# Kernel optimization log

Measured on AMD Instinct MI355X. Metric: run time of the kernel, lower is better.

Reference implementation:

```python
import jax, jax.numpy as jnp
import numpy as np

ONE_STEP = 14
EPS = 1e-5


def _bn(x, g, b):
    # training-mode batchnorm over the node/batch axis (biased variance)
    m = jnp.mean(x, axis=0)
    v = jnp.var(x, axis=0)
    return (x - m) * jax.lax.rsqrt(v + EPS) * g + b


def _gcn_conv(x, W, b, src, dst, dis):
    N = x.shape[0]
    h = x @ W
    norm = (dis[src] * dis[dst])[:, None]
    agg = jax.ops.segment_sum(h[src] * norm, dst, num_segments=N)
    agg = agg + (dis * dis)[:, None] * h  # self-loop contribution
    return agg + b


def setup_inputs() -> dict:
    key = jax.random.key(0)
    ks = jax.random.split(key, 16)
    N, F, E, NC = 114688, 512, 917504, 10
    x = jax.random.normal(ks[0], (N, F), jnp.float32)
    edge_index = jax.random.randint(ks[1], (2, E), 0, N, jnp.int32)

    def lin(k, i, o):
        return jax.random.normal(k, (i, o), jnp.float32) / np.sqrt(i).astype(np.float32)

    d = {"x": x, "edge_index": edge_index}
    dims = [(F, 128), (128, 256), (256, 64), (64, 32)]
    for li, (i, o) in enumerate(dims, 1):
        d[f"W{li}"] = lin(ks[1 + li], i, o)
        d[f"b{li}"] = jnp.zeros((o,), jnp.float32)
        d[f"bn{li}_g"] = jnp.ones((o,), jnp.float32)
        d[f"bn{li}_b"] = jnp.zeros((o,), jnp.float32)
    d["gW1"] = lin(ks[6], 32, 16); d["gb1"] = jnp.zeros((16,), jnp.float32)
    d["gbn1_g"] = jnp.ones((16,), jnp.float32); d["gbn1_b"] = jnp.zeros((16,), jnp.float32)
    d["gW2"] = lin(ks[7], 16, 1); d["gb2"] = jnp.zeros((1,), jnp.float32)
    d["gbn2_g"] = jnp.ones((1,), jnp.float32); d["gbn2_b"] = jnp.zeros((1,), jnp.float32)
    d["fcW"] = lin(ks[8], 32, NC); d["fcb"] = jnp.zeros((NC,), jnp.float32)
    return d


def reference(x, edge_index, W1, b1, bn1_g, bn1_b, W2, b2, bn2_g, bn2_b,
              W3, b3, bn3_g, bn3_b, W4, b4, bn4_g, bn4_b,
              gW1, gb1, gbn1_g, gbn1_b, gW2, gb2, gbn2_g, gbn2_b, fcW, fcb):
    N = x.shape[0]
    src, dst = edge_index[0], edge_index[1]
    # degree with self-loops (counted on dst, per PyG gcn_norm)
    deg = jax.ops.segment_sum(jnp.ones_like(dst, jnp.float32), dst, num_segments=N) + 1.0
    dis = jax.lax.rsqrt(deg)

    h = _bn(jax.nn.relu(_gcn_conv(x, W1, b1, src, dst, dis)), bn1_g, bn1_b)
    h = _bn(jax.nn.relu(_gcn_conv(h, W2, b2, src, dst, dis)), bn2_g, bn2_b)
    h = _bn(jax.nn.relu(_gcn_conv(h, W3, b3, src, dst, dis)), bn3_g, bn3_b)
    h = _bn(jax.nn.relu(_gcn_conv(h, W4, b4, src, dst, dis)), bn4_g, bn4_b)

    # gate network: Linear -> BN -> ReLU -> Linear -> BN -> ReLU
    g = jax.nn.relu(_bn(h @ gW1 + gb1, gbn1_g, gbn1_b))
    g = jax.nn.relu(_bn(g @ gW2 + gb2, gbn2_g, gbn2_b))[:, 0]  # [N]

    B = N // ONE_STEP
    batch = jnp.repeat(jnp.arange(B), ONE_STEP)
    # segment softmax over nodes of each graph
    m = jax.ops.segment_max(g, batch, num_segments=B)
    e = jnp.exp(g - m[batch])
    s = jax.ops.segment_sum(e, batch, num_segments=B)
    alpha = e / s[batch]
    pooled = jax.ops.segment_sum(alpha[:, None] * h, batch, num_segments=B)  # [B,32]

    # dropout is identity in eval mode
    logits = pooled @ fcW + fcb
    return jax.nn.softmax(logits, axis=1)
```

## Files before the change

### kernel.cpp

```cpp
#include <hip/hip_runtime.h>

#define NN 114688
#define NE 917504
#define NBATCH 8192
#define GSZ 14
#define NCLS 10
#define EPSB 1e-5f
#define NSCAN 112

typedef unsigned short u16;
typedef short bf16x8 __attribute__((ext_vector_type(8)));
typedef float f32x4 __attribute__((ext_vector_type(4)));
typedef _Float16 h8t __attribute__((ext_vector_type(8)));
typedef unsigned short u16x8 __attribute__((ext_vector_type(8)));

__device__ __forceinline__ float bf2f(u16 u) {
    union { unsigned int i; float f; } v; v.i = ((unsigned int)u) << 16; return v.f;
}
__device__ __forceinline__ u16 f2bf(float f) {
    union { float f; unsigned int i; } v; v.f = f;
    unsigned int i = v.i;
    unsigned int r = i + 0x7FFFu + ((i >> 16) & 1u);
    return (u16)(r >> 16);
}
__device__ __forceinline__ void splitbf(float y, u16& h, u16& l) {
    h = f2bf(y);
    l = f2bf(y - bf2f(h));
}

__global__ __launch_bounds__(256) void k_hist(const int* __restrict__ ei, int* __restrict__ counts) {
    int e = blockIdx.x * 256 + threadIdx.x;
    atomicAdd(&counts[ei[NE + e]], 1);
}

__global__ __launch_bounds__(256) void k_scan1(const int* __restrict__ counts, int* __restrict__ bsum) {
    __shared__ int red[256];
    int tid = threadIdx.x;
    int base = blockIdx.x * 1024 + tid * 4;
    int s = counts[base] + counts[base + 1] + counts[base + 2] + counts[base + 3];
    red[tid] = s; __syncthreads();
    for (int o = 128; o > 0; o >>= 1) {
        if (tid < o) red[tid] += red[tid + o];
        __syncthreads();
    }
    if (tid == 0) bsum[blockIdx.x] = red[0];
}

__global__ void k_scan2(int* bsum, int* offs) {
    if (threadIdx.x == 0) {
        int run = 0;
        for (int i = 0; i < NSCAN; i++) { int t = bsum[i]; bsum[i] = run; run += t; }
        offs[NN] = run;
    }
}

__global__ __launch_bounds__(256) void k_scan3(const int* __restrict__ counts, const int* __restrict__ bsum,
                                               int* __restrict__ offs) {
    __shared__ int ss[256];
    int tid = threadIdx.x;
    int base = blockIdx.x * 1024 + tid * 4;
    int v0 = counts[base], v1 = counts[base + 1], v2 = counts[base + 2], v3 = counts[base + 3];
    int ts = v0 + v1 + v2 + v3;
    ss[tid] = ts; __syncthreads();
    for (int o = 1; o < 256; o <<= 1) {
        int add = (tid >= o) ? ss[tid - o] : 0;
        __syncthreads();
        ss[tid] += add;
        __syncthreads();
    }
    int excl = ss[tid] - ts + bsum[blockIdx.x];
    offs[base] = excl;
    offs[base + 1] = excl + v0;
    offs[base + 2] = excl + v0 + v1;
    offs[base + 3] = excl + v0 + v1 + v2;
}

__global__ __launch_bounds__(256) void k_dis_cursor(const int* __restrict__ counts, const int* __restrict__ offs,
                                                    float* __restrict__ dis, int* __restrict__ cursor) {
    int n = blockIdx.x * 256 + threadIdx.x;
    dis[n] = rsqrtf((float)counts[n] + 1.0f);
    cursor[n] = offs[n];
}

__global__ __launch_bounds__(256) void k_scatter(const int* __restrict__ ei, int* __restrict__ cursor,
                                                 int* __restrict__ srcs, float* __restrict__ sd,
                                                 const float* __restrict__ dis, float* __restrict__ wsa) {
    int e = blockIdx.x * 256 + threadIdx.x;
    int d = ei[NE + e], s = ei[e];
    int p = atomicAdd(&cursor[d], 1);
    float w = dis[s];
    srcs[p] = s;
    sd[p] = w;
    atomicAdd(&wsa[d], w);
}

__global__ __launch_bounds__(256) void k_tsplit(const float* __restrict__ Wsrc,
                                                u16* __restrict__ Wh, u16* __restrict__ Wl,
                                                int K, int F) {
    int i = blockIdx.x * 256 + threadIdx.x;
    if (i < K * F) {
        int k = i / F, f = i % F;
        u16 h, l; splitbf(Wsrc[i], h, l);
        Wh[f * K + k] = h;
        Wl[f * K + k] = l;
    }
}

__global__ __launch_bounds__(256) void k_wsplit(const float* __restrict__ W, const float* __restrict__ sc,
                                                u16* __restrict__ Wh, u16* __restrict__ Wl,
                                                int K, int F) {
    int i = blockIdx.x * 256 + threadIdx.x;
    if (i < K * F) {
        int k = i / F, f = i % F;
        u16 h, l; splitbf(sc[k] * W[i], h, l);
        Wh[f * K + k] = h;
        Wl[f * K + k] = l;
    }
}

__global__ __launch_bounds__(256) void k_wc2(const float* __restrict__ W, const float* __restrict__ sh,
                                             float* __restrict__ c2, int K, int F) {
    int wv = (blockIdx.x * 256 + threadIdx.x) >> 6;
    int lane = threadIdx.x & 63;
    if (wv >= F) return;
    float acc = 0.f;
    for (int k = lane; k < K; k += 64) acc += sh[k] * W[k * F + wv];
#pragma unroll
    for (int o = 1; o < 64; o <<= 1) acc += __shfl_xor(acc, o);
    if (lane == 0) c2[wv] = acc;
}

template<int BM, int BN, int WCOLS, bool AFP32, bool C2, bool TEPI>
__global__ __launch_bounds__(256) void k_gemm(
    const float* __restrict__ Af, const u16* __restrict__ Ahi, const u16* __restrict__ Alo,
    const u16* __restrict__ Wh, const u16* __restrict__ Wl,
    _Float16* __restrict__ C, const int K, const int Fout, const float* __restrict__ c2,
    const float* __restrict__ bias, const float* __restrict__ wsa, const float* __restrict__ disv,
    u16* __restrict__ Thi, u16* __restrict__ Tlo, float* __restrict__ Sg, float* __restrict__ Qg)
{
    constexpr int AST = 40;
    __shared__ u16 Ah[BM][AST], Al[BM][AST];
    __shared__ u16 Bh[BN][AST], Bl[BN][AST];
    __shared__ float redS[TEPI ? BN : 1], redQ[TEPI ? BN : 1];

    const int tid = threadIdx.x;
    const int row0 = blockIdx.y * BM;
    const int col0 = blockIdx.x * BN;

    const int wave = tid >> 6, lane = tid & 63;
    const int mb = (wave / WCOLS) * 64;
    const int nb = (wave % WCOLS) * 64;
    const int lm = lane & 15;
    const int lk = (lane >> 4) * 8;
    const int cb = col0 + nb + lm;

    if constexpr (TEPI) {
        for (int i = tid; i < BN; i += 256) { redS[i] = 0.f; redQ[i] = 0.f; }
    }

    float c2v[4] = {0.f, 0.f, 0.f, 0.f};
    if constexpr (C2) {
#pragma unroll
        for (int ni = 0; ni < 4; ni++) c2v[ni] = c2[cb + ni * 16];
    }

    f32x4 acc[4][4];
#pragma unroll
    for (int i = 0; i < 4; i++)
#pragma unroll
        for (int j = 0; j < 4; j++)
#pragma unroll
            for (int r = 0; r < 4; r++) acc[i][j][r] = c2v[j];

    const int stg_r = tid >> 3;
    const int stg_c = (tid & 7) * 4;

    for (int k0 = 0; k0 < K; k0 += 32) {
        __syncthreads();
#pragma unroll
        for (int p = 0; p < BM / 32; p++) {
            const int r = p * 32 + stg_r;
            if constexpr (AFP32) {
                const float4 v = *(const float4*)(Af + (size_t)(row0 + r) * K + k0 + stg_c);
                float y[4] = {v.x, v.y, v.z, v.w};
                ushort4 hv, lv;
#pragma unroll
                for (int q = 0; q < 4; q++) splitbf(y[q], ((u16*)&hv)[q], ((u16*)&lv)[q]);
                *(ushort4*)&Ah[r][stg_c] = hv;
                *(ushort4*)&Al[r][stg_c] = lv;
            } else {
                *(ushort4*)&Ah[r][stg_c] = *(const ushort4*)(Ahi + (size_t)(row0 + r) * K + k0 + stg_c);
                *(ushort4*)&Al[r][stg_c] = *(const ushort4*)(Alo + (size_t)(row0 + r) * K + k0 + stg_c);
            }
        }
#pragma unroll
        for (int p = 0; p < BN / 32; p++) {
            const int n = p * 32 + stg_r;
            *(ushort4*)&Bh[n][stg_c] = *(const ushort4*)(Wh + (size_t)(col0 + n) * K + k0 + stg_c);
            *(ushort4*)&Bl[n][stg_c] = *(const ushort4*)(Wl + (size_t)(col0 + n) * K + k0 + stg_c);
        }
        __syncthreads();

        bf16x8 ah[4], al[4], bh[4], bl[4];
#pragma unroll
        for (int mi = 0; mi < 4; mi++) {
            ah[mi] = *(const bf16x8*)&Ah[mb + mi * 16 + lm][lk];
            al[mi] = *(const bf16x8*)&Al[mb + mi * 16 + lm][lk];
        }
#pragma unroll
        for (int ni = 0; ni < 4; ni++) {
            bh[ni] = *(const bf16x8*)&Bh[nb + ni * 16 + lm][lk];
            bl[ni] = *(const bf16x8*)&Bl[nb + ni * 16 + lm][lk];
        }
#pragma unroll
        for (int mi = 0; mi < 4; mi++)
#pragma unroll
            for (int ni = 0; ni < 4; ni++) {
                acc[mi][ni] = __builtin_amdgcn_mfma_f32_16x16x32_bf16(al[mi], bh[ni], acc[mi][ni], 0, 0, 0);
                acc[mi][ni] = __builtin_amdgcn_mfma_f32_16x16x32_bf16(ah[mi], bl[ni], acc[mi][ni], 0, 0, 0);
                acc[mi][ni] = __builtin_amdgcn_mfma_f32_16x16x32_bf16(ah[mi], bh[ni], acc[mi][ni], 0, 0, 0);
            }
    }

    const int rb = row0 + mb + (lane >> 4) * 4;
    if constexpr (TEPI) {
        float c2l[4], bl4[4];
#pragma unroll
        for (int ni = 0; ni < 4; ni++) { c2l[ni] = c2[cb + ni * 16]; bl4[ni] = bias[cb + ni * 16]; }
        float ws[4][4];
#pragma unroll
        for (int mi = 0; mi < 4; mi++)
#pragma unroll
            for (int r = 0; r < 4; r++) {
                const int row = rb + mi * 16 + r;
                const float d = disv[row];
                ws[mi][r] = d * wsa[row] + d * d;
            }
#pragma unroll
        for (int ni = 0; ni < 4; ni++) {
            float s = 0.f, q = 0.f;
#pragma unroll
            for (int mi = 0; mi < 4; mi++)
#pragma unroll
                for (int r = 0; r < 4; r++) {
                    float v = acc[mi][ni][r] + ws[mi][r] * c2l[ni] + bl4[ni];
                    v = fmaxf(v, 0.f);
                    s += v; q += v * v;
                    u16 hh, ll; splitbf(v, hh, ll);
                    const size_t idx = (size_t)(rb + mi * 16 + r) * Fout + cb + ni * 16;
                    Thi[idx] = hh;
                    Tlo[idx] = ll;
                }
            atomicAdd(&redS[nb + ni * 16 + lm], s);
            atomicAdd(&redQ[nb + ni * 16 + lm], q);
        }
        __syncthreads();
        for (int i = tid; i < BN; i += 256) {
            atomicAdd(&Sg[col0 + i], redS[i]);
            atomicAdd(&Qg[col0 + i], redQ[i]);
        }
    } else {
#pragma unroll
        for (int mi = 0; mi < 4; mi++)
#pragma unroll
            for (int ni = 0; ni < 4; ni++)
#pragma unroll
                for (int r = 0; r < 4; r++)
                    C[(size_t)(rb + mi * 16 + r) * Fout + cb + ni * 16] = (_Float16)acc[mi][ni][r];
    }
}

template<int CH, bool FP16OUT>
__global__ __launch_bounds__(256) void k_agg(
    const _Float16* __restrict__ h, u16* __restrict__ thi, u16* __restrict__ tlo,
    const float* __restrict__ bias,
    const int* __restrict__ off, const int* __restrict__ srcs, const float* __restrict__ sd,
    const float* __restrict__ dis, float* __restrict__ statS, float* __restrict__ statQ,
    _Float16* __restrict__ tf)
{
    constexpr int ECH = 16;
    constexpr int LPG = CH / ECH;
    constexpr int G   = 64 / LPG;
    constexpr int NB  = NN / G;
    __shared__ float redS[CH], redQ[CH];
    const int tid = threadIdx.x;
    for (int i = tid; i < CH; i += 256) { redS[i] = 0.f; redQ[i] = 0.f; }
    __syncthreads();

    const int lane = tid & 63;
    const int g = lane / LPG;
    const int c = (lane % LPG) * ECH;
    const int wid = (blockIdx.x * 256 + tid) >> 6;
    const int nw = (gridDim.x * 256) >> 6;

    float bs[ECH], bq[ECH], bv[ECH];
#pragma unroll
    for (int v = 0; v < ECH; v++) { bs[v] = 0.f; bq[v] = 0.f; bv[v] = bias[c + v]; }

    for (int b = wid; b < NB; b += nw) {
        const int n = b * G + g;
        const int p0 = off[n], p1 = off[n + 1];
        float a[ECH];
#pragma unroll
        for (int v = 0; v < ECH; v++) a[v] = 0.f;

        int p = p0;
        int s = 0; float w = 0.f;
        if (p < p1) { s = srcs[p]; w = sd[p]; }
        while (p < p1) {
            int s2 = 0; float w2 = 0.f;
            if (p + 1 < p1) { s2 = srcs[p + 1]; w2 = sd[p + 1]; }
            const _Float16* hr = h + (size_t)s * CH + c;
            h8t hv0 = *(const h8t*)hr;
            h8t hv1 = *(const h8t*)(hr + 8);
#pragma unroll
            for (int v = 0; v < 8; v++) { a[v] += w * (float)hv0[v]; a[v + 8] += w * (float)hv1[v]; }
            s = s2; w = w2; ++p;
        }
        const float dn = dis[n];
        const float dn2 = dn * dn;
        const _Float16* hr = h + (size_t)n * CH + c;
        h8t hn0 = *(const h8t*)hr;
        h8t hn1 = *(const h8t*)(hr + 8);
        float o16[ECH];
#pragma unroll
        for (int v = 0; v < 8; v++) {
            o16[v] = fmaxf(dn * a[v] + dn2 * (float)hn0[v] + bv[v], 0.f);
            o16[v + 8] = fmaxf(dn * a[v + 8] + dn2 * (float)hn1[v] + bv[v + 8], 0.f);
        }
#pragma unroll
        for (int v = 0; v < ECH; v++) { bs[v] += o16[v]; bq[v] += o16[v] * o16[v]; }
        if constexpr (FP16OUT) {
            h8t o0, o1;
#pragma unroll
            for (int v = 0; v < 8; v++) { o0[v] = (_Float16)o16[v]; o1[v] = (_Float16)o16[v + 8]; }
            _Float16* tr = tf + (size_t)n * CH + c;
            *(h8t*)tr = o0; *(h8t*)(tr + 8) = o1;
        } else {
            u16x8 hv0, lv0, hv1, lv1;
#pragma unroll
            for (int v = 0; v < 8; v++) {
                splitbf(o16[v], ((u16*)&hv0)[v], ((u16*)&lv0)[v]);
                splitbf(o16[v + 8], ((u16*)&hv1)[v], ((u16*)&lv1)[v]);
            }
            u16* th = thi + (size_t)n * CH + c;
            u16* tl = tlo + (size_t)n * CH + c;
            *(u16x8*)th = hv0; *(u16x8*)(th + 8) = hv1;
            *(u16x8*)tl = lv0; *(u16x8*)(tl + 8) = lv1;
        }
    }
#pragma unroll
    for (int o = LPG; o < 64; o <<= 1) {
#pragma unroll
        for (int v = 0; v < ECH; v++) { bs[v] += __shfl_xor(bs[v], o); bq[v] += __shfl_xor(bq[v], o); }
    }
    if (g == 0) {
#pragma unroll
        for (int v = 0; v < ECH; v++) { atomicAdd(&redS[c + v], bs[v]); atomicAdd(&redQ[c + v], bq[v]); }
    }
    __syncthreads();
    for (int i = tid; i < CH; i += 256) { atomicAdd(&statS[i], redS[i]); atomicAdd(&statQ[i], redQ[i]); }
}

template<int CH>
__global__ __launch_bounds__(256) void k_agglin(
    const _Float16* __restrict__ t, u16* __restrict__ uhi, u16* __restrict__ ulo,
    const int* __restrict__ off, const int* __restrict__ srcs, const float* __restrict__ sd,
    const float* __restrict__ dis)
{
    constexpr int ECH = 16;
    constexpr int LPG = CH / ECH;
    constexpr int G   = 64 / LPG;
    constexpr int NB  = NN / G;
    const int tid = threadIdx.x;
    const int lane = tid & 63;
    const int g = lane / LPG;
    const int c = (lane % LPG) * ECH;
    const int wid = (blockIdx.x * 256 + tid) >> 6;
    const int nw = (gridDim.x * 256) >> 6;

    for (int b = wid; b < NB; b += nw) {
        const int n = b * G + g;
        const int p0 = off[n], p1 = off[n + 1];
        float a[ECH];
#pragma unroll
        for (int v = 0; v < ECH; v++) a[v] = 0.f;

        int p = p0;
        int s = 0; float w = 0.f;
        if (p < p1) { s = srcs[p]; w = sd[p]; }
        while (p < p1) {
            int s2 = 0; float w2 = 0.f;
            if (p + 1 < p1) { s2 = srcs[p + 1]; w2 = sd[p + 1]; }
            const _Float16* hr = t + (size_t)s * CH + c;
            h8t hv0 = *(const h8t*)hr;
            h8t hv1 = *(const h8t*)(hr + 8);
#pragma unroll
            for (int v = 0; v < 8; v++) { a[v] += w * (float)hv0[v]; a[v + 8] += w * (float)hv1[v]; }
            s = s2; w = w2; ++p;
        }
        const float dn = dis[n];
        const float dn2 = dn * dn;
        const _Float16* hr = t + (size_t)n * CH + c;
        h8t hn0 = *(const h8t*)hr;
        h8t hn1 = *(const h8t*)(hr + 8);
        u16x8 hv0, lv0, hv1, lv1;
#pragma unroll
        for (int v = 0; v < 8; v++) {
            float o0 = dn * a[v] + dn2 * (float)hn0[v];
            float o1 = dn * a[v + 8] + dn2 * (float)hn1[v];
            splitbf(o0, ((u16*)&hv0)[v], ((u16*)&lv0)[v]);
            splitbf(o1, ((u16*)&hv1)[v], ((u16*)&lv1)[v]);
        }
        u16* th = uhi + (size_t)n * CH + c;
        u16* tl = ulo + (size_t)n * CH + c;
        *(u16x8*)th = hv0; *(u16x8*)(th + 8) = hv1;
        *(u16x8*)tl = lv0; *(u16x8*)(tl + 8) = lv1;
    }
}

__global__ void k_bnpar(const float* __restrict__ S, const float* __restrict__ Q,
                        const float* __restrict__ g, const float* __restrict__ b,
                        float* __restrict__ sc, float* __restrict__ sh, int F) {
    int c = threadIdx.x;
    if (c >= F) return;
    const float invn = 1.0f / (float)NN;
    float mean = S[c] * invn;
    float var = Q[c] * invn - mean * mean;
    float s = g[c] * rsqrtf(fmaxf(var, 0.f) + EPSB);
    sc[c] = s;
    sh[c] = b[c] - mean * s;
}

template<int K, int F, bool BIAS, bool STATS>
__global__ __launch_bounds__(256) void k_smm(
    const u16* __restrict__ Ahi, const u16* __restrict__ Alo,
    const float* __restrict__ Wf, const float* __restrict__ bias,
    _Float16* __restrict__ C, const float* __restrict__ sc, const float* __restrict__ sh,
    float* __restrict__ Sg, float* __restrict__ Qg)
{
    __shared__ float Wl[K * F];
    __shared__ float scl[K], shl[K], bl[F];
    __shared__ float redS[F], redQ[F];
    const int tid = threadIdx.x;
    for (int i = tid; i < K * F; i += 256) Wl[i] = Wf[i];
    if (tid < K) { scl[tid] = sc[tid]; shl[tid] = sh[tid]; }
    if (tid < F) {
        bl[tid] = 0.f;
        if constexpr (BIAS) bl[tid] = bias[tid];
        if constexpr (STATS) { redS[tid] = 0.f; redQ[tid] = 0.f; }
    }
    __syncthreads();
    const int n = blockIdx.x * 256 + tid;
    float acc[F];
#pragma unroll
    for (int f = 0; f < F; f++) acc[f] = bl[f];
    const u16* ah = Ahi + (size_t)n * K;
    const u16* al = Alo + (size_t)n * K;
    for (int k = 0; k < K; k += 4) {
        ushort4 hv = *(const ushort4*)(ah + k);
        ushort4 lv = *(const ushort4*)(al + k);
        float y0 = (bf2f(hv.x) + bf2f(lv.x)) * scl[k] + shl[k];
        float y1 = (bf2f(hv.y) + bf2f(lv.y)) * scl[k + 1] + shl[k + 1];
        float y2 = (bf2f(hv.z) + bf2f(lv.z)) * scl[k + 2] + shl[k + 2];
        float y3 = (bf2f(hv.w) + bf2f(lv.w)) * scl[k + 3] + shl[k + 3];
#pragma unroll
        for (int f = 0; f < F; f += 4) {
            float4 w0 = *(const float4*)&Wl[k * F + f];
            float4 w1 = *(const float4*)&Wl[(k + 1) * F + f];
            float4 w2 = *(const float4*)&Wl[(k + 2) * F + f];
            float4 w3 = *(const float4*)&Wl[(k + 3) * F + f];
            acc[f + 0] += y0 * w0.x + y1 * w1.x + y2 * w2.x + y3 * w3.x;
            acc[f + 1] += y0 * w0.y + y1 * w1.y + y2 * w2.y + y3 * w3.y;
            acc[f + 2] += y0 * w0.z + y1 * w1.z + y2 * w2.z + y3 * w3.z;
            acc[f + 3] += y0 * w0.w + y1 * w1.w + y2 * w2.w + y3 * w3.w;
        }
    }
    _Float16* cr = C + (size_t)n * F;
#pragma unroll
    for (int f = 0; f < F; f++) cr[f] = (_Float16)acc[f];
    if constexpr (STATS) {
        float s[F], q[F];
#pragma unroll
        for (int f = 0; f < F; f++) { s[f] = acc[f]; q[f] = acc[f] * acc[f]; }
#pragma unroll
        for (int o = 1; o < 64; o <<= 1) {
#pragma unroll
            for (int f = 0; f < F; f++) { s[f] += __shfl_xor(s[f], o); q[f] += __shfl_xor(q[f], o); }
        }
        if ((tid & 63) == 0) {
#pragma unroll
            for (int f = 0; f < F; f++) { atomicAdd(&redS[f], s[f]); atomicAdd(&redQ[f], q[f]); }
        }
        __syncthreads();
        for (int i = tid; i < F; i += 256) { atomicAdd(&Sg[i], redS[i]); atomicAdd(&Qg[i], redQ[i]); }
    }
}

__global__ __launch_bounds__(256) void k_gate2(const _Float16* __restrict__ g1,
                                               const float* __restrict__ sc, const float* __restrict__ sh,
                                               const float* __restrict__ w2, const float* __restrict__ b2,
                                               float* __restrict__ g2,
                                               float* __restrict__ Sg, float* __restrict__ Qg) {
    __shared__ float wl[16], scl[16], shl[16], b2l[1];
    __shared__ float redSg[1], redQg[1];
    const int tid = threadIdx.x;
    if (tid < 16) { wl[tid] = w2[tid]; scl[tid] = sc[tid]; shl[tid] = sh[tid]; }
    if (tid == 0) { b2l[0] = b2[0]; redSg[0] = 0.f; redQg[0] = 0.f; }
    __syncthreads();
    const int n = blockIdx.x * 256 + tid;
    const _Float16* r = g1 + (size_t)n * 16;
    float acc = b2l[0];
#pragma unroll
    for (int k = 0; k < 16; k++) {
        float y = fmaxf((float)r[k] * scl[k] + shl[k], 0.f);
        acc += y * wl[k];
    }
    g2[n] = acc;
    float s = acc, q = acc * acc;
#pragma unroll
    for (int o = 1; o < 64; o <<= 1) { s += __shfl_xor(s, o); q += __shfl_xor(q, o); }
    if ((tid & 63) == 0) { atomicAdd(&redSg[0], s); atomicAdd(&redQg[0], q); }
    __syncthreads();
    if (tid == 0) { atomicAdd(&Sg[0], redSg[0]); atomicAdd(&Qg[0], redQg[0]); }
}

__global__ __launch_bounds__(256) void k_pool(const u16* __restrict__ t4hi, const u16* __restrict__ t4lo,
                                              const float* __restrict__ sc4, const float* __restrict__ sh4,
                                              const float* __restrict__ g2,
                                              const float* __restrict__ gsc2, const float* __restrict__ gsh2,
                                              const float* __restrict__ fcW, const float* __restrict__ fcb,
                                              float* __restrict__ out) {
    __shared__ float fw[32 * NCLS], fbl[NCLS], sc4l[32], sh4l[32];
    const int tid = threadIdx.x;
    for (int i = tid; i < 32 * NCLS; i += 256) fw[i] = fcW[i];
    if (tid < NCLS) fbl[tid] = fcb[tid];
    if (tid < 32) { sc4l[tid] = sc4[tid]; sh4l[tid] = sh4[tid]; }
    __syncthreads();
    const int b = blockIdx.x * 256 + tid;
    const float s2 = gsc2[0], h2 = gsh2[0];
    const int base = b * GSZ;

    float gv[GSZ];
    float m = -1e30f;
#pragma unroll
    for (int i = 0; i < GSZ; i++) {
        float v = fmaxf(g2[base + i] * s2 + h2, 0.f);
        gv[i] = v; m = fmaxf(m, v);
    }
    float ssum = 0.f;
#pragma unroll
    for (int i = 0; i < GSZ; i++) { float e = __expf(gv[i] - m); gv[i] = e; ssum += e; }
    const float inv = 1.0f / ssum;

    float pooled[32];
#pragma unroll
    for (int c = 0; c < 32; c++) pooled[c] = 0.f;
#pragma unroll
    for (int i = 0; i < GSZ; i++) {
        const float a = gv[i] * inv;
        const u16* th = t4hi + (size_t)(base + i) * 32;
        const u16* tl = t4lo + (size_t)(base + i) * 32;
#pragma unroll
        for (int c = 0; c < 32; c += 4) {
            ushort4 hv = *(const ushort4*)(th + c);
            ushort4 lv = *(const ushort4*)(tl + c);
            pooled[c + 0] += a * ((bf2f(hv.x) + bf2f(lv.x)) * sc4l[c + 0] + sh4l[c + 0]);
            pooled[c + 1] += a * ((bf2f(hv.y) + bf2f(lv.y)) * sc4l[c + 1] + sh4l[c + 1]);
            pooled[c + 2] += a * ((bf2f(hv.z) + bf2f(lv.z)) * sc4l[c + 2] + sh4l[c + 2]);
            pooled[c + 3] += a * ((bf2f(hv.w) + bf2f(lv.w)) * sc4l[c + 3] + sh4l[c + 3]);
        }
    }
    float lg[NCLS];
    float mx = -1e30f;
#pragma unroll
    for (int j = 0; j < NCLS; j++) {
        float a = fbl[j];
#pragma unroll
        for (int c = 0; c < 32; c++) a += pooled[c] * fw[c * NCLS + j];
        lg[j] = a; mx = fmaxf(mx, a);
    }
    float es = 0.f;
#pragma unroll
    for (int j = 0; j < NCLS; j++) { float e = __expf(lg[j] - mx); lg[j] = e; es += e; }
    const float iv = 1.0f / es;
#pragma unroll
    for (int j = 0; j < NCLS; j++) out[b * NCLS + j] = lg[j] * iv;
}

extern "C" void kernel_launch(void* const* d_in, const int* in_sizes, int n_in,
                              void* d_out, int out_size, void* d_ws, size_t ws_size,
                              hipStream_t stream) {
    (void)in_sizes; (void)n_in; (void)out_size; (void)ws_size;
    const float* x    = (const float*)d_in[0];
    const int*   ei   = (const int*)d_in[1];
    const float* W1   = (const float*)d_in[2];
    const float* b1   = (const float*)d_in[3];
    const float* bn1g = (const float*)d_in[4];
    const float* bn1b = (const float*)d_in[5];
    const float* W2   = (const float*)d_in[6];
    const float* b2   = (const float*)d_in[7];
    const float* bn2g = (const float*)d_in[8];
    const float* bn2b = (const float*)d_in[9];
    const float* W3   = (const float*)d_in[10];
    const float* b3   = (const float*)d_in[11];
    const float* bn3g = (const float*)d_in[12];
    const float* bn3b = (const float*)d_in[13];
    const float* W4   = (const float*)d_in[14];
    const float* b4   = (const float*)d_in[15];
    const float* bn4g = (const float*)d_in[16];
    const float* bn4b = (const float*)d_in[17];
    const float* gW1  = (const float*)d_in[18];
    const float* gb1  = (const float*)d_in[19];
    const float* gbn1g = (const float*)d_in[20];
    const float* gbn1b = (const float*)d_in[21];
    const float* gW2  = (const float*)d_in[22];
    const float* gb2  = (const float*)d_in[23];
    const float* gbn2g = (const float*)d_in[24];
    const float* gbn2b = (const float*)d_in[25];
    const float* fcW  = (const float*)d_in[26];
    const float* fcb  = (const float*)d_in[27];
    float* out = (float*)d_out;

    char* base = (char*)d_ws;
    size_t off_ = 0;
    auto carve = [&](size_t bytes) -> char* {
        char* p = base + off_;
        off_ = (off_ + bytes + 255) & ~(size_t)255;
        return p;
    };
    int*   counts = (int*)carve((size_t)NN * 4);
    float* stats  = (float*)carve(994 * 4);
    float* wsa    = (float*)carve((size_t)NN * 4);
    const size_t zero_bytes = off_;
    int*   offs   = (int*)carve((size_t)(NN + 1) * 4);
    int*   cursor = (int*)carve((size_t)NN * 4);
    int*   srcs   = (int*)carve((size_t)NE * 4);
    float* sd     = (float*)carve((size_t)NE * 4);
    float* dis    = (float*)carve((size_t)NN * 4);
    int*   bsum   = (int*)carve(NSCAN * 4);
    float* pars   = (float*)carve(994 * 4);
    u16*   Wt1h   = (u16*)carve(512 * 128 * 2);
    u16*   Wt1l   = (u16*)carve(512 * 128 * 2);
    u16*   Wt2h   = (u16*)carve(128 * 256 * 2);
    u16*   Wt2l   = (u16*)carve(128 * 256 * 2);
    u16*   Wt3h   = (u16*)carve(256 * 64 * 2);
    u16*   Wt3l   = (u16*)carve(256 * 64 * 2);
    float* c2_2   = (float*)carve(256 * 4);
    float* c2_3   = (float*)carve(64 * 4);
    float* g2raw  = (float*)carve((size_t)NN * 4);
    _Float16* P   = (_Float16*)carve((size_t)NN * 256 * 2);
    u16*   Qhi    = (u16*)carve((size_t)NN * 128 * 2);
    u16*   Qlo    = (u16*)carve((size_t)NN * 128 * 2);
    u16*   Rhi    = (u16*)carve((size_t)NN * 256 * 2);
    u16*   Rlo    = (u16*)carve((size_t)NN * 256 * 2);
    _Float16* T1f = P + (size_t)NN * 128;

    float* S1 = stats;      float* Q1s = S1 + 128;
    float* S2 = Q1s + 128;  float* Q2s = S2 + 256;
    float* S3 = Q2s + 256;  float* Q3s = S3 + 64;
    float* S4 = Q3s + 64;   float* Q4s = S4 + 32;
    float* gS1 = Q4s + 32;  float* gQ1 = gS1 + 16;
    float* gS2 = gQ1 + 16;  float* gQ2 = gS2 + 1;

    float* sc1 = pars;      float* sh1 = sc1 + 128;
    float* sc2 = sh1 + 128; float* sh2 = sc2 + 256;
    float* sc3 = sh2 + 256; float* sh3 = sc3 + 64;
    float* sc4 = sh3 + 64;  float* sh4 = sc4 + 32;
    float* gsc1 = sh4 + 32; float* gsh1 = gsc1 + 16;
    float* gsc2 = gsh1 + 16; float* gsh2 = gsc2 + 1;

    hipMemsetAsync(d_ws, 0, zero_bytes, stream);

    k_hist<<<NE / 256, 256, 0, stream>>>(ei, counts);
    k_scan1<<<NSCAN, 256, 0, stream>>>(counts, bsum);
    k_scan2<<<1, 64, 0, stream>>>(bsum, offs);
    k_scan3<<<NSCAN, 256, 0, stream>>>(counts, bsum, offs);
    k_dis_cursor<<<NN / 256, 256, 0, stream>>>(counts, offs, dis, cursor);
    k_scatter<<<NE / 256, 256, 0, stream>>>(ei, cursor, srcs, sd, dis, wsa);
    k_tsplit<<<(512 * 128 + 255) / 256, 256, 0, stream>>>(W1, Wt1h, Wt1l, 512, 128);

    k_gemm<128, 128, 2, true, false, false><<<dim3(1, NN / 128), 256, 0, stream>>>(
        x, nullptr, nullptr, Wt1h, Wt1l, P, 512, 128, nullptr,
        nullptr, nullptr, nullptr, nullptr, nullptr, nullptr, nullptr);
    k_agg<128, true><<<1792, 256, 0, stream>>>(P, nullptr, nullptr, b1, offs, srcs, sd, dis, S1, Q1s, T1f);
    k_bnpar<<<1, 256, 0, stream>>>(S1, Q1s, bn1g, bn1b, sc1, sh1, 128);

    k_agglin<128><<<1792, 256, 0, stream>>>(T1f, Qhi, Qlo, offs, srcs, sd, dis);
    k_wsplit<<<(128 * 256 + 255) / 256, 256, 0, stream>>>(W2, sc1, Wt2h, Wt2l, 128, 256);
    k_wc2<<<(256 * 64 + 255) / 256, 256, 0, stream>>>(W2, sh1, c2_2, 128, 256);
    k_gemm<128, 128, 2, false, false, true><<<dim3(2, NN / 128), 256, 0, stream>>>(
        nullptr, Qhi, Qlo, Wt2h, Wt2l, nullptr, 128, 256, c2_2,
        b2, wsa, dis, Rhi, Rlo, S2, Q2s);
    k_bnpar<<<1, 256, 0, stream>>>(S2, Q2s, bn2g, bn2b, sc2, sh2, 256);

    k_wsplit<<<(256 * 64 + 255) / 256, 256, 0, stream>>>(W3, sc2, Wt3h, Wt3l, 256, 64);
    k_wc2<<<(64 * 64 + 255) / 256, 256, 0, stream>>>(W3, sh2, c2_3, 256, 64);
    k_gemm<256, 64, 1, false, true, false><<<dim3(1, NN / 256), 256, 0, stream>>>(
        nullptr, Rhi, Rlo, Wt3h, Wt3l, P, 256, 64, c2_3,
        nullptr, nullptr, nullptr, nullptr, nullptr, nullptr, nullptr);
    k_agg<64, false><<<1792, 256, 0, stream>>>(P, Qhi, Qlo, b3, offs, srcs, sd, dis, S3, Q3s, nullptr);
    k_bnpar<<<1, 256, 0, stream>>>(S3, Q3s, bn3g, bn3b, sc3, sh3, 64);

    k_smm<64, 32, false, false><<<NN / 256, 256, 0, stream>>>(Qhi, Qlo, W4, nullptr, P, sc3, sh3,
                                                              nullptr, nullptr);
    k_agg<32, false><<<896, 256, 0, stream>>>(P, Qhi, Qlo, b4, offs, srcs, sd, dis, S4, Q4s, nullptr);
    k_bnpar<<<1, 256, 0, stream>>>(S4, Q4s, bn4g, bn4b, sc4, sh4, 32);

    k_smm<32, 16, true, true><<<NN / 256, 256, 0, stream>>>(Qhi, Qlo, gW1, gb1, P, sc4, sh4, gS1, gQ1);
    k_bnpar<<<1, 256, 0, stream>>>(gS1, gQ1, gbn1g, gbn1b, gsc1, gsh1, 16);

    k_gate2<<<NN / 256, 256, 0, stream>>>(P, gsc1, gsh1, gW2, gb2, g2raw, gS2, gQ2);
    k_bnpar<<<1, 256, 0, stream>>>(gS2, gQ2, gbn2g, gbn2b, gsc2, gsh2, 1);

    k_pool<<<NBATCH / 256, 256, 0, stream>>>(Qhi, Qlo, sc4, sh4, g2raw, gsc2, gsh2, fcW, fcb, out);
}
```

Baseline: 974.9 us.

## Fold BN parameter kernels into consumers, fuse dis/cursor into scan, unroll gather

Removes the six tiny k_bnpar launches by computing batchnorm scale/shift inline in each consuming kernel from the raw sum and sum-of-squares. It also folds the dis/cursor initialisation into k_scan3, and unrolls the edge-gather loops in the aggregation kernels by two so each iteration has two independent row loads in flight. The goal is fewer kernel launches and more memory-level parallelism in the gathers. In exchange, some BN parameter math is recomputed redundantly per thread, for example inside k_wsplit and k_wc2.

```diff
diff --git a/kernel.cpp b/kernel.cpp
--- a/kernel.cpp
+++ b/kernel.cpp
@@ -26,6 +26,16 @@
 __device__ __forceinline__ void splitbf(float y, u16& h, u16& l) {
     h = f2bf(y);
     l = f2bf(y - bf2f(h));
+}
+__device__ __forceinline__ void bnparams(const float* __restrict__ S, const float* __restrict__ Q,
+                                         const float* __restrict__ g, const float* __restrict__ b,
+                                         int c, float& sc, float& sh) {
+    const float invn = 1.0f / (float)NN;
+    float mean = S[c] * invn;
+    float var = Q[c] * invn - mean * mean;
+    float s = g[c] * rsqrtf(fmaxf(var, 0.f) + EPSB);
+    sc = s;
+    sh = b[c] - mean * s;
 }
 
 __global__ __launch_bounds__(256) void k_hist(const int* __restrict__ ei, int* __restrict__ counts) {
@@ -55,7 +65,8 @@
 }
 
 __global__ __launch_bounds__(256) void k_scan3(const int* __restrict__ counts, const int* __restrict__ bsum,
-                                               int* __restrict__ offs) {
+                                               int* __restrict__ offs, float* __restrict__ dis,
+                                               int* __restrict__ cursor) {
     __shared__ int ss[256];
     int tid = threadIdx.x;
     int base = blockIdx.x * 1024 + tid * 4;
@@ -69,17 +80,13 @@
         __syncthreads();
     }
     int excl = ss[tid] - ts + bsum[blockIdx.x];
-    offs[base] = excl;
-    offs[base + 1] = excl + v0;
-    offs[base + 2] = excl + v0 + v1;
-    offs[base + 3] = excl + v0 + v1 + v2;
-}
-
-__global__ __launch_bounds__(256) void k_dis_cursor(const int* __restrict__ counts, const int* __restrict__ offs,
-                                                    float* __restrict__ dis, int* __restrict__ cursor) {
-    int n = blockIdx.x * 256 + threadIdx.x;
-    dis[n] = rsqrtf((float)counts[n] + 1.0f);
-    cursor[n] = offs[n];
+    int o0 = excl, o1 = excl + v0, o2 = o1 + v1, o3 = o2 + v2;
+    offs[base] = o0; offs[base + 1] = o1; offs[base + 2] = o2; offs[base + 3] = o3;
+    cursor[base] = o0; cursor[base + 1] = o1; cursor[base + 2] = o2; cursor[base + 3] = o3;
+    dis[base]     = rsqrtf((float)v0 + 1.0f);
+    dis[base + 1] = rsqrtf((float)v1 + 1.0f);
+    dis[base + 2] = rsqrtf((float)v2 + 1.0f);
+    dis[base + 3] = rsqrtf((float)v3 + 1.0f);
 }
 
 __global__ __launch_bounds__(256) void k_scatter(const int* __restrict__ ei, int* __restrict__ cursor,
@@ -106,25 +113,33 @@
     }
 }
 
-__global__ __launch_bounds__(256) void k_wsplit(const float* __restrict__ W, const float* __restrict__ sc,
+__global__ __launch_bounds__(256) void k_wsplit(const float* __restrict__ W,
+                                                const float* __restrict__ S, const float* __restrict__ Q,
+                                                const float* __restrict__ g, const float* __restrict__ b,
                                                 u16* __restrict__ Wh, u16* __restrict__ Wl,
                                                 int K, int F) {
     int i = blockIdx.x * 256 + threadIdx.x;
     if (i < K * F) {
         int k = i / F, f = i % F;
-        u16 h, l; splitbf(sc[k] * W[i], h, l);
+        float sc, sh; bnparams(S, Q, g, b, k, sc, sh);
+        u16 h, l; splitbf(sc * W[i], h, l);
         Wh[f * K + k] = h;
         Wl[f * K + k] = l;
     }
 }
 
-__global__ __launch_bounds__(256) void k_wc2(const float* __restrict__ W, const float* __restrict__ sh,
+__global__ __launch_bounds__(256) void k_wc2(const float* __restrict__ W,
+                                             const float* __restrict__ S, const float* __restrict__ Q,
+                                             const float* __restrict__ g, const float* __restrict__ b,
                                              float* __restrict__ c2, int K, int F) {
     int wv = (blockIdx.x * 256 + threadIdx.x) >> 6;
     int lane = threadIdx.x & 63;
     if (wv >= F) return;
     float acc = 0.f;
-    for (int k = lane; k < K; k += 64) acc += sh[k] * W[k * F + wv];
+    for (int k = lane; k < K; k += 64) {
+        float sc, sh; bnparams(S, Q, g, b, k, sc, sh);
+        acc += sh * W[k * F + wv];
+    }
 #pragma unroll
     for (int o = 1; o < 64; o <<= 1) acc += __shfl_xor(acc, o);
     if (lane == 0) c2[wv] = acc;
@@ -305,17 +320,30 @@
         for (int v = 0; v < ECH; v++) a[v] = 0.f;
 
         int p = p0;
-        int s = 0; float w = 0.f;
-        if (p < p1) { s = srcs[p]; w = sd[p]; }
-        while (p < p1) {
-            int s2 = 0; float w2 = 0.f;
-            if (p + 1 < p1) { s2 = srcs[p + 1]; w2 = sd[p + 1]; }
-            const _Float16* hr = h + (size_t)s * CH + c;
-            h8t hv0 = *(const h8t*)hr;
-            h8t hv1 = *(const h8t*)(hr + 8);
-#pragma unroll
-            for (int v = 0; v < 8; v++) { a[v] += w * (float)hv0[v]; a[v + 8] += w * (float)hv1[v]; }
-            s = s2; w = w2; ++p;
+        while (p + 2 <= p1) {
+            const int sA = srcs[p], sB = srcs[p + 1];
+            const float wA = sd[p], wB = sd[p + 1];
+            const _Float16* hA = h + (size_t)sA * CH + c;
+            const _Float16* hB = h + (size_t)sB * CH + c;
+            h8t a0 = *(const h8t*)hA;
+            h8t a1 = *(const h8t*)(hA + 8);
+            h8t b0 = *(const h8t*)hB;
+            h8t b1 = *(const h8t*)(hB + 8);
+#pragma unroll
+            for (int v = 0; v < 8; v++) {
+                a[v]     += wA * (float)a0[v] + wB * (float)b0[v];
+                a[v + 8] += wA * (float)a1[v] + wB * (float)b1[v];
+            }
+            p += 2;
+        }
+        if (p < p1) {
+            const int sA = srcs[p];
+            const float wA = sd[p];
+            const _Float16* hA = h + (size_t)sA * CH + c;
+            h8t a0 = *(const h8t*)hA;
+            h8t a1 = *(const h8t*)(hA + 8);
+#pragma unroll
+            for (int v = 0; v < 8; v++) { a[v] += wA * (float)a0[v]; a[v + 8] += wA * (float)a1[v]; }
         }
         const float dn = dis[n];
         const float dn2 = dn * dn;
@@ -387,17 +415,30 @@
         for (int v = 0; v < ECH; v++) a[v] = 0.f;
 
         int p = p0;
-        int s = 0; float w = 0.f;
-        if (p < p1) { s = srcs[p]; w = sd[p]; }
-        while (p < p1) {
-            int s2 = 0; float w2 = 0.f;
-            if (p + 1 < p1) { s2 = srcs[p + 1]; w2 = sd[p + 1]; }
-            const _Float16* hr = t + (size_t)s * CH + c;
-            h8t hv0 = *(const h8t*)hr;
-            h8t hv1 = *(const h8t*)(hr + 8);
-#pragma unroll
-            for (int v = 0; v < 8; v++) { a[v] += w * (float)hv0[v]; a[v + 8] += w * (float)hv1[v]; }
-            s = s2; w = w2; ++p;
+        while (p + 2 <= p1) {
+            const int sA = srcs[p], sB = srcs[p + 1];
+            const float wA = sd[p], wB = sd[p + 1];
+            const _Float16* hA = t + (size_t)sA * CH + c;
+            const _Float16* hB = t + (size_t)sB * CH + c;
+            h8t a0 = *(const h8t*)hA;
+            h8t a1 = *(const h8t*)(hA + 8);
+            h8t b0 = *(const h8t*)hB;
+            h8t b1 = *(const h8t*)(hB + 8);
+#pragma unroll
+            for (int v = 0; v < 8; v++) {
+                a[v]     += wA * (float)a0[v] + wB * (float)b0[v];
+                a[v + 8] += wA * (float)a1[v] + wB * (float)b1[v];
+            }
+            p += 2;
+        }
+        if (p < p1) {
+            const int sA = srcs[p];
+            const float wA = sd[p];
+            const _Float16* hA = t + (size_t)sA * CH + c;
+            h8t a0 = *(const h8t*)hA;
+            h8t a1 = *(const h8t*)(hA + 8);
+#pragma unroll
+            for (int v = 0; v < 8; v++) { a[v] += wA * (float)a0[v]; a[v + 8] += wA * (float)a1[v]; }
         }
         const float dn = dis[n];
         const float dn2 = dn * dn;
@@ -419,24 +460,13 @@
     }
 }
 
-__global__ void k_bnpar(const float* __restrict__ S, const float* __restrict__ Q,
-                        const float* __restrict__ g, const float* __restrict__ b,
-                        float* __restrict__ sc, float* __restrict__ sh, int F) {
-    int c = threadIdx.x;
-    if (c >= F) return;
-    const float invn = 1.0f / (float)NN;
-    float mean = S[c] * invn;
-    float var = Q[c] * invn - mean * mean;
-    float s = g[c] * rsqrtf(fmaxf(var, 0.f) + EPSB);
-    sc[c] = s;
-    sh[c] = b[c] - mean * s;
-}
-
 template<int K, int F, bool BIAS, bool STATS>
 __global__ __launch_bounds__(256) void k_smm(
     const u16* __restrict__ Ahi, const u16* __restrict__ Alo,
     const float* __restrict__ Wf, const float* __restrict__ bias,
-    _Float16* __restrict__ C, const float* __restrict__ sc, const float* __restrict__ sh,
+    _Float16* __restrict__ C,
+    const float* __restrict__ Sb, const float* __restrict__ Qb,
+    const float* __restrict__ gb, const float* __restrict__ bb,
     float* __restrict__ Sg, float* __restrict__ Qg)
 {
     __shared__ float Wl[K * F];
@@ -444,7 +474,10 @@
     __shared__ float redS[F], redQ[F];
     const int tid = threadIdx.x;
     for (int i = tid; i < K * F; i += 256) Wl[i] = Wf[i];
-    if (tid < K) { scl[tid] = sc[tid]; shl[tid] = sh[tid]; }
+    if (tid < K) {
+        float s, h_; bnparams(Sb, Qb, gb, bb, tid, s, h_);
+        scl[tid] = s; shl[tid] = h_;
+    }
     if (tid < F) {
         bl[tid] = 0.f;
         if constexpr (BIAS) bl[tid] = bias[tid];
@@ -498,14 +531,19 @@
 }
 
 __global__ __launch_bounds__(256) void k_gate2(const _Float16* __restrict__ g1,
-                                               const float* __restrict__ sc, const float* __restrict__ sh,
+                                               const float* __restrict__ S1g, const float* __restrict__ Q1g,
+                                               const float* __restrict__ gg, const float* __restrict__ gbb,
                                                const float* __restrict__ w2, const float* __restrict__ b2,
                                                float* __restrict__ g2,
                                                float* __restrict__ Sg, float* __restrict__ Qg) {
     __shared__ float wl[16], scl[16], shl[16], b2l[1];
     __shared__ float redSg[1], redQg[1];
     const int tid = threadIdx.x;
-    if (tid < 16) { wl[tid] = w2[tid]; scl[tid] = sc[tid]; shl[tid] = sh[tid]; }
+    if (tid < 16) {
+        wl[tid] = w2[tid];
+        float s, h_; bnparams(S1g, Q1g, gg, gbb, tid, s, h_);
+        scl[tid] = s; shl[tid] = h_;
+    }
     if (tid == 0) { b2l[0] = b2[0]; redSg[0] = 0.f; redQg[0] = 0.f; }
     __syncthreads();
     const int n = blockIdx.x * 256 + tid;
@@ -526,19 +564,28 @@
 }
 
 __global__ __launch_bounds__(256) void k_pool(const u16* __restrict__ t4hi, const u16* __restrict__ t4lo,
-                                              const float* __restrict__ sc4, const float* __restrict__ sh4,
+                                              const float* __restrict__ S4, const float* __restrict__ Q4,
+                                              const float* __restrict__ g4, const float* __restrict__ b4,
                                               const float* __restrict__ g2,
-                                              const float* __restrict__ gsc2, const float* __restrict__ gsh2,
+                                              const float* __restrict__ gS2, const float* __restrict__ gQ2,
+                                              const float* __restrict__ gg2, const float* __restrict__ gbb2,
                                               const float* __restrict__ fcW, const float* __restrict__ fcb,
                                               float* __restrict__ out) {
-    __shared__ float fw[32 * NCLS], fbl[NCLS], sc4l[32], sh4l[32];
+    __shared__ float fw[32 * NCLS], fbl[NCLS], sc4l[32], sh4l[32], g2p[2];
     const int tid = threadIdx.x;
     for (int i = tid; i < 32 * NCLS; i += 256) fw[i] = fcW[i];
     if (tid < NCLS) fbl[tid] = fcb[tid];
-    if (tid < 32) { sc4l[tid] = sc4[tid]; sh4l[tid] = sh4[tid]; }
+    if (tid < 32) {
+        float s, h_; bnparams(S4, Q4, g4, b4, tid, s, h_);
+        sc4l[tid] = s; sh4l[tid] = h_;
+    }
+    if (tid == 0) {
+        float s, h_; bnparams(gS2, gQ2, gg2, gbb2, 0, s, h_);
+        g2p[0] = s; g2p[1] = h_;
+    }
     __syncthreads();
     const int b = blockIdx.x * 256 + tid;
-    const float s2 = gsc2[0], h2 = gsh2[0];
+    const float s2 = g2p[0], h2 = g2p[1];
     const int base = b * GSZ;
 
     float gv[GSZ];
@@ -639,7 +686,6 @@
     float* sd     = (float*)carve((size_t)NE * 4);
     float* dis    = (float*)carve((size_t)NN * 4);
     int*   bsum   = (int*)carve(NSCAN * 4);
-    float* pars   = (float*)carve(994 * 4);
     u16*   Wt1h   = (u16*)carve(512 * 128 * 2);
     u16*   Wt1l   = (u16*)carve(512 * 128 * 2);
     u16*   Wt2h   = (u16*)carve(128 * 256 * 2);
@@ -663,20 +709,12 @@
     float* gS1 = Q4s + 32;  float* gQ1 = gS1 + 16;
     float* gS2 = gQ1 + 16;  float* gQ2 = gS2 + 1;
 
-    float* sc1 = pars;      float* sh1 = sc1 + 128;
-    float* sc2 = sh1 + 128; float* sh2 = sc2 + 256;
-    float* sc3 = sh2 + 256; float* sh3 = sc3 + 64;
-    float* sc4 = sh3 + 64;  float* sh4 = sc4 + 32;
-    float* gsc1 = sh4 + 32; float* gsh1 = gsc1 + 16;
-    float* gsc2 = gsh1 + 16; float* gsh2 = gsc2 + 1;
-
     hipMemsetAsync(d_ws, 0, zero_bytes, stream);
 
     k_hist<<<NE / 256, 256, 0, stream>>>(ei, counts);
     k_scan1<<<NSCAN, 256, 0, stream>>>(counts, bsum);
     k_scan2<<<1, 64, 0, stream>>>(bsum, offs);
-    k_scan3<<<NSCAN, 256, 0, stream>>>(counts, bsum, offs);
-    k_dis_cursor<<<NN / 256, 256, 0, stream>>>(counts, offs, dis, cursor);
+    k_scan3<<<NSCAN, 256, 0, stream>>>(counts, bsum, offs, dis, cursor);
     k_scatter<<<NE / 256, 256, 0, stream>>>(ei, cursor, srcs, sd, dis, wsa);
     k_tsplit<<<(512 * 128 + 255) / 256, 256, 0, stream>>>(W1, Wt1h, Wt1l, 512, 128);
 
@@ -684,34 +722,30 @@
         x, nullptr, nullptr, Wt1h, Wt1l, P, 512, 128, nullptr,
         nullptr, nullptr, nullptr, nullptr, nullptr, nullptr, nullptr);
     k_agg<128, true><<<1792, 256, 0, stream>>>(P, nullptr, nullptr, b1, offs, srcs, sd, dis, S1, Q1s, T1f);
-    k_bnpar<<<1, 256, 0, stream>>>(S1, Q1s, bn1g, bn1b, sc1, sh1, 128);
 
     k_agglin<128><<<1792, 256, 0, stream>>>(T1f, Qhi, Qlo, offs, srcs, sd, dis);
-    k_wsplit<<<(128 * 256 + 255) / 256, 256, 0, stream>>>(W2, sc1, Wt2h, Wt2l, 128, 256);
-    k_wc2<<<(256 * 64 + 255) / 256, 256, 0, stream>>>(W2, sh1, c2_2, 128, 256);
+    k_wsplit<<<(128 * 256 + 255) / 256, 256, 0, stream>>>(W2, S1, Q1s, bn1g, bn1b, Wt2h, Wt2l, 128, 256);
+    k_wc2<<<(256 * 64 + 255) / 256, 256, 0, stream>>>(W2, S1, Q1s, bn1g, bn1b, c2_2, 128, 256);
     k_gemm<128, 128, 2, false, false, true><<<dim3(2, NN / 128), 256, 0, stream>>>(
         nullptr, Qhi, Qlo, Wt2h, Wt2l, nullptr, 128, 256, c2_2,
         b2, wsa, dis, Rhi, Rlo, S2, Q2s);
-    k_bnpar<<<1, 256, 0, stream>>>(S2, Q2s, bn2g, bn2b, sc2, sh2, 256);
-
-    k_wsplit<<<(256 * 64 + 255) / 256, 256, 0, stream>>>(W3, sc2, Wt3h, Wt3l, 256, 64);
-    k_wc2<<<(64 * 64 + 255) / 256, 256, 0, stream>>>(W3, sh2, c2_3, 256, 64);
+
+    k_wsplit<<<(256 * 64 + 255) / 256, 256, 0, stream>>>(W3, S2, Q2s, bn2g, bn2b, Wt3h, Wt3l, 256, 64);
+    k_wc2<<<(64 * 64 + 255) / 256, 256, 0, stream>>>(W3, S2, Q2s, bn2g, bn2b, c2_3, 256, 64);
     k_gemm<256, 64, 1, false, true, false><<<dim3(1, NN / 256), 256, 0, stream>>>(
         nullptr, Rhi, Rlo, Wt3h, Wt3l, P, 256, 64, c2_3,
         nullptr, nullptr, nullptr, nullptr, nullptr, nullptr, nullptr);
     k_agg<64, false><<<1792, 256, 0, stream>>>(P, Qhi, Qlo, b3, offs, srcs, sd, dis, S3, Q3s, nullptr);
-    k_bnpar<<<1, 256, 0, stream>>>(S3, Q3s, bn3g, bn3b, sc3, sh3, 64);
-
-    k_smm<64, 32, false, false><<<NN / 256, 256, 0, stream>>>(Qhi, Qlo, W4, nullptr, P, sc3, sh3,
-                                                              nullptr, nullptr);
+
+    k_smm<64, 32, false, false><<<NN / 256, 256, 0, stream>>>(Qhi, Qlo, W4, nullptr, P,
+                                                              S3, Q3s, bn3g, bn3b, nullptr, nullptr);
     k_agg<32, false><<<896, 256, 0, stream>>>(P, Qhi, Qlo, b4, offs, srcs, sd, dis, S4, Q4s, nullptr);
-    k_bnpar<<<1, 256, 0, stream>>>(S4, Q4s, bn4g, bn4b, sc4, sh4, 32);
-
-    k_smm<32, 16, true, true><<<NN / 256, 256, 0, stream>>>(Qhi, Qlo, gW1, gb1, P, sc4, sh4, gS1, gQ1);
-    k_bnpar<<<1, 256, 0, stream>>>(gS1, gQ1, gbn1g, gbn1b, gsc1, gsh1, 16);
-
-    k_gate2<<<NN / 256, 256, 0, stream>>>(P, gsc1, gsh1, gW2, gb2, g2raw, gS2, gQ2);
-    k_bnpar<<<1, 256, 0, stream>>>(gS2, gQ2, gbn2g, gbn2b, gsc2, gsh2, 1);
-
-    k_pool<<<NBATCH / 256, 256, 0, stream>>>(Qhi, Qlo, sc4, sh4, g2raw, gsc2, gsh2, fcW, fcb, out);
-}
+
+    k_smm<32, 16, true, true><<<NN / 256, 256, 0, stream>>>(Qhi, Qlo, gW1, gb1, P,
+                                                            S4, Q4s, bn4g, bn4b, gS1, gQ1);
+
+    k_gate2<<<NN / 256, 256, 0, stream>>>(P, gS1, gQ1, gbn1g, gbn1b, gW2, gb2, g2raw, gS2, gQ2);
+
+    k_pool<<<NBATCH / 256, 256, 0, stream>>>(Qhi, Qlo, S4, Q4s, bn4g, bn4b,
+                                             g2raw, gS2, gQ2, gbn2g, gbn2b, fcW, fcb, out);
+}
```

After: 956.7 us. About the same (-1.9%).
